# Performance work log

Hardware: AMD Instinct MI355X
Metric: run time of the kernel (lower is better)

Reference implementation:

```python
import jax, jax.numpy as jnp
import numpy as np
from jax.scipy.special import erf

# ---- physical constants (scipy.constants values; FIELD_CONSTANT in eV*Angstrom per e^2) ----
E_CHARGE = 1.602176634e-19
EPS0 = 8.8541878128e-12
PI = float(np.pi)
FIELD_CONSTANT = E_CHARGE * 1e10 / EPS0          # e/(eps0) with Angstrom length units
K_COUL = FIELD_CONSTANT / (4.0 * PI)             # ~14.3996 eV*A

# ---- module hyperparameters (from init_kwargs) ----
SIGMA_D = 0.5
SIGMAS = np.array([0.4, 0.8, 1.2, 1.6], dtype=np.float32)
NUM_RADIAL = 4
OFFSET = 0.1
N_PER_GRAPH = 128
NUM_GRAPHS = 32
M_NODES = N_PER_GRAPH * NUM_GRAPHS

# total_width_factors = sqrt((sigma_d^2 + sigma_r^2)/2)
W_FACTORS = np.sqrt((SIGMA_D**2 + SIGMAS**2) / 2.0).astype(np.float32)      # [R]
# multipole-normalized GTO: C_l = 1/(2^{l+1/2} sigma^{2l+3} Gamma(l+3/2)) => C1/C0 = 1/(3 sigma^2)
L0_FACTORS = np.ones(NUM_RADIAL, dtype=np.float32)                          # ratio = 1 under 'multipoles'
L1_FACTORS = (np.sqrt(3.0) * SIGMAS**2 * (1.0 / (3.0 * SIGMAS**2)) / OFFSET).astype(np.float32)

# 7 duplicate offsets: center, +x, +y, +z, -x, -y, -z
_h = OFFSET
OFFSETS7 = np.array([[0,0,0],[_h,0,0],[0,_h,0],[0,0,_h],[-_h,0,0],[0,-_h,0],[0,0,-_h]], dtype=np.float32)


def _duplicate_charges(sf):
    # sf: [M,4] -> [M,7] FD charge assignment (matches torch slot layout)
    t = 2.0 * OFFSET
    s0, s1, s2, s3 = sf[:, 0], sf[:, 1], sf[:, 2], sf[:, 3]
    return jnp.stack([s0, s3 / t, s1 / t, s2 / t, -s3 / t, -s1 / t, -s2 / t], axis=1)


def _project(sf7):
    # sf7: [M,7,R] per-duplicate scalar features -> [M, 4R]
    M = sf7.shape[0]
    l0 = jnp.asarray(L0_FACTORS) * sf7[:, 0]                                 # [M,R]
    half = 0.5 * jnp.asarray(L1_FACTORS)
    vy = half * (sf7[:, 2] - sf7[:, 5])   # column offset 0 in each triplet
    vz = half * (sf7[:, 3] - sf7[:, 6])   # column offset 1
    vx = half * (sf7[:, 1] - sf7[:, 4])   # column offset 2
    l1 = jnp.stack([vy, vz, vx], axis=-1).reshape(M, 3 * NUM_RADIAL)         # interleaved per radial
    return jnp.concatenate([l0, l1], axis=1)                                 # [M,4R]


def setup_inputs() -> dict:
    key = jax.random.key(0)
    k1, k2 = jax.random.split(key)
    source_feats = jax.random.normal(k1, (M_NODES, 1, 4), dtype=jnp.float32)
    node_positions = 4.0 * jax.random.normal(k2, (M_NODES, 3), dtype=jnp.float32)  # ~Angstrom scale
    batch = jnp.repeat(jnp.arange(NUM_GRAPHS, dtype=jnp.int64), N_PER_GRAPH)
    return {"source_feats": source_feats, "node_positions": node_positions, "batch": batch}


def reference(source_feats, node_positions, batch):
    # density_max_l=1, projection_max_l=1 -> call_density_1_feats_1 path.
    # Assumes equal-size graphs: batch = repeat(arange(G), n) (enforced by setup_inputs).
    sf = source_feats[:, 0, :]                                               # squeeze(-2): [M,4]
    M = sf.shape[0]
    G, n, D, R = NUM_GRAPHS, N_PER_GRAPH, 7 * N_PER_GRAPH, NUM_RADIAL
    w = jnp.asarray(W_FACTORS)                                               # [R]

    charges = _duplicate_charges(sf)                                         # [M,7]
    pos7 = node_positions[:, None, :] + jnp.asarray(OFFSETS7)[None]          # [M,7,3]

    pg = pos7.reshape(G, D, 3)
    cg = charges.reshape(G, D)

    diff = pg[:, :, None, :] - pg[:, None, :, :]                             # [G,D,D,3]
    d2 = jnp.sum(diff * diff, axis=-1)                                       # [G,D,D]
    orig = jnp.arange(D) // 7
    mask = (orig[:, None] != orig[None, :])                                  # exclude same-original-node pairs
    d = jnp.sqrt(jnp.where(mask, d2, 1.0))                                   # safe sqrt (masked entries dummy)
    smooth = erf(0.5 * d[..., None] / w) / (d[..., None] + 1e-6)             # [G,D,D,R]
    smooth = smooth * mask[None, :, :, None]
    # scatter_sum over senders i into receivers j
    sfeat = K_COUL * jnp.einsum('gi,gijr->gjr', cg, smooth)                  # [G,D,R]
    sfeat = sfeat.reshape(M, 7, R)

    # GTOSelfInteractionBlock (reconstructed): interactions among a node's own
    # 7 duplicates with analytic d->0 limit erf(x)/x -> 1/(w*sqrt(pi)).
    off = jnp.asarray(OFFSETS7)
    ds = jnp.linalg.norm(off[:, None, :] - off[None, :, :], axis=-1)          # [7,7]
    phi = jnp.where(ds[..., None] > 0.0,
                    erf(0.5 * ds[..., None] / w) / (ds[..., None] + 1e-6),
                    1.0 / (w * np.sqrt(PI)))                                  # [7,7,R]
    sself = K_COUL * jnp.einsum('mi,ijr->mjr', charges, phi)                  # [M,7,R]

    features = _project(sfeat)
    self_terms = _project(sself)
    features = features + self_terms                                          # include_self_interaction=True
    return features, self_terms
```

## Files before the change

kernel.cpp:

```cpp
#include <hip/hip_runtime.h>
#include <math.h>

namespace {

constexpr int   MTOT = 4096;
constexpr float H    = 0.1f;

constexpr float W0 = 0.45276925690687087f;
constexpr float W1 = 0.66708320320631664f;
constexpr float W2 = 0.91923881554251174f;
constexpr float W3 = 1.18532695911296985f;

constexpr float KCOUL   = 14.399645478425669f;
constexpr float HALF_L1 = 2.8867513459481287f;
constexpr float SQRTPI  = 1.7724538509055159f;
constexpr float TWOSQPI = 1.1283791670955126f;

constexpr float K0 = 1.1043153f, K1 = 0.74953184f, K2 = 0.54392830f, K3 = 0.42182454f;

constexpr float PK0 = 0.5195472f, PK1 = 0.3526314f, PK2 = 0.2559019f, PK3 = 0.1984558f;
constexpr float C20 = -1.7593842f, C21 = -0.8105028f, C22 = -0.4268329f, C23 = -0.2567073f;
constexpr float EA1 = 0.3480242f, EA2 = -0.0958798f, EA3 = 0.7478556f;
constexpr float RCP_H = 9.9999000f, RCP_HS2 = 7.0710178f, RCP_2H = 4.9999750f;

constexpr int   TABN  = 512;
constexpr float TAB_H = 0.015f;
constexpr float INV_H = 66.666664f;

constexpr int   TGN   = 256;
constexpr float TG_H  = 0.03f;
constexpr float INV_G = 33.333332f;

constexpr float NEAR2 = 4.0f;
constexpr float SAT2  = 49.4f;

__device__ __forceinline__ float fast_rcp(float x)  { return __builtin_amdgcn_rcpf(x); }
__device__ __forceinline__ float fast_rsq(float x)  { return __builtin_amdgcn_rsqf(x); }
__device__ __forceinline__ float fast_exp2(float x) { return __builtin_amdgcn_exp2f(x); }

__device__ __forceinline__ float erf_q(float d, float d2, float pk, float c2) {
  float t = fast_rcp(__builtin_fmaf(d, pk, 1.0f));
  float poly = t * __builtin_fmaf(t, __builtin_fmaf(t, EA3, EA2), EA1);
  return poly * fast_exp2(d2 * c2);
}

__device__ __forceinline__ float project_one(const float* S, int k) {
  if (k < 4) return S[k];
  int q = k - 4;
  int r = q / 3;
  int comp = q - 3 * r;
  int j1, j2;
  if (comp == 0)      { j1 = 2; j2 = 5; }
  else if (comp == 1) { j1 = 3; j2 = 6; }
  else                { j1 = 1; j2 = 4; }
  return HALF_L1 * (S[j1 * 4 + r] - S[j2 * 4 + r]);
}

__device__ __forceinline__ unsigned spread3(int v) {
  return (unsigned)((v & 1) | ((v & 2) << 2) | ((v & 4) << 4));
}

__global__ __launch_bounds__(896, 4) void es_main(
    const float* __restrict__ sf,
    const float* __restrict__ pos,
    float* __restrict__ out)
{
  __shared__ float4   s_pos4[128];
  __shared__ float4   s_chg4[128];
  __shared__ int      s_orig[128];
  __shared__ unsigned s_key[128];
  __shared__ float4   s_tabV[TABN];
  __shared__ float4   s_tabD[TABN];
  __shared__ float4   s_gV[TGN], s_gD[TGN];
  __shared__ float4   s_tV[TGN], s_tD[TGN];
  __shared__ __align__(16) char s_u[8 * 112 * 16];
  __shared__ float    s_feat[448];
  __shared__ float    s_self[448];

  float (*s_tmp)[TABN + 1] = reinterpret_cast<float (*)[TABN + 1]>(s_u);
  float4* s_part = reinterpret_cast<float4*>(s_u);

  const int b   = blockIdx.x;
  const int g   = b >> 3;
  const int nb  = b & 7;
  const int tid = threadIdx.x;

  float px = 0.f, py = 0.f, pz = 0.f;
  float4 myc = make_float4(0.f, 0.f, 0.f, 0.f);
  if (tid < 128) {
    const float* p = pos + (size_t)(g * 128 + tid) * 3;
    px = p[0]; py = p[1]; pz = p[2];
    const float4 s = ((const float4*)sf)[g * 128 + tid];
    myc = make_float4(s.x, 5.0f * s.w, 5.0f * s.y, 5.0f * s.z);
    int cx = (int)((px + 16.0f) * 0.25f); cx = (cx < 0) ? 0 : (cx > 7 ? 7 : cx);
    int cy = (int)((py + 16.0f) * 0.25f); cy = (cy < 0) ? 0 : (cy > 7 ? 7 : cy);
    int cz = (int)((pz + 16.0f) * 0.25f); cz = (cz < 0) ? 0 : (cz > 7 ? 7 : cz);
    unsigned mort = spread3(cx) | (spread3(cy) << 1) | (spread3(cz) << 2);
    s_key[tid] = (mort << 7) | (unsigned)tid;
  }
  if (tid <= TABN) {
    const float d = tid * TAB_H;
    s_tmp[0][tid] = erff(K0 * d);
    s_tmp[1][tid] = erff(K1 * d);
    s_tmp[2][tid] = erff(K2 * d);
    s_tmp[3][tid] = erff(K3 * d);
  }
  if (tid >= 640) {
    const int e = tid - 640;
    const float d0 = fmaxf(e * TG_H, 1e-3f);
    const float d1 = (e + 1) * TG_H;
    const float ks[4] = {K0, K1, K2, K3};
    float gv[4], gd[4], tv[4], td[4];
#pragma unroll
    for (int r = 0; r < 4; ++r) {
      const float k = ks[r];
      const float e0 = erff(k * d0), e1 = erff(k * d1);
      const float x0 = expf(-k * k * d0 * d0), x1 = expf(-k * k * d1 * d1);
      const float g0 = e0 / d0, g1 = e1 / d1;
      const float t0 = 0.2f * e0 / (d0 * d0 * d0) - 0.2f * TWOSQPI * k * x0 / (d0 * d0);
      const float t1 = 0.2f * e1 / (d1 * d1 * d1) - 0.2f * TWOSQPI * k * x1 / (d1 * d1);
      gv[r] = g0; gd[r] = g1 - g0; tv[r] = t0; td[r] = t1 - t0;
    }
    s_gV[e] = make_float4(gv[0], gv[1], gv[2], gv[3]);
    s_gD[e] = make_float4(gd[0], gd[1], gd[2], gd[3]);
    s_tV[e] = make_float4(tv[0], tv[1], tv[2], tv[3]);
    s_tD[e] = make_float4(td[0], td[1], td[2], td[3]);
  }
  __syncthreads();

  if (tid < 128) {
    const unsigned mykey = s_key[tid];
    int rank = 0;
    for (int t = 0; t < 128; ++t) rank += (s_key[t] < mykey) ? 1 : 0;
    s_pos4[rank] = make_float4(px, py, pz, 0.0f);
    s_chg4[rank] = myc;
    s_orig[rank] = tid;
  }
  if (tid < TABN) {
    const float v0 = s_tmp[0][tid], v1 = s_tmp[1][tid];
    const float v2v = s_tmp[2][tid], v3 = s_tmp[3][tid];
    s_tabV[tid] = make_float4(v0, v1, v2v, v3);
    s_tabD[tid] = make_float4(s_tmp[0][tid + 1] - v0, s_tmp[1][tid + 1] - v1,
                              s_tmp[2][tid + 1] - v2v, s_tmp[3][tid + 1] - v3);
  }
  __syncthreads();

  const int site_local = tid % 112;
  const int chunk      = tid / 112;
  const int sl   = nb * 112 + site_local;
  const int jown = (sl * 9363) >> 16;
  const int aoff = sl - jown * 7;

  const float4 cp = s_pos4[jown];
  const float tx = cp.x + ((aoff == 1) ? H : (aoff == 4) ? -H : 0.0f);
  const float ty = cp.y + ((aoff == 2) ? H : (aoff == 5) ? -H : 0.0f);
  const float tz = cp.z + ((aoff == 3) ? H : (aoff == 6) ? -H : 0.0f);

  float a0 = 0.f, a1 = 0.f, a2 = 0.f, a3 = 0.f, Ssat = 0.f;

  auto acc_full = [&](float d2raw, float c) {
    float d2 = fmaxf(d2raw, 1e-12f);
    float rd = fast_rsq(d2);
    float cv = c * rd;
    float t  = (d2 * rd) * INV_H;
    int  idx = (int)t;
    float f  = t - (float)idx;
    idx = (idx < TABN - 1) ? idx : (TABN - 1);
    f = fminf(f, 1.0f);
    const float4 V = s_tabV[idx];
    const float4 D = s_tabD[idx];
    a0 = __builtin_fmaf(cv, __builtin_fmaf(D.x, f, V.x), a0);
    a1 = __builtin_fmaf(cv, __builtin_fmaf(D.y, f, V.y), a1);
    a2 = __builtin_fmaf(cv, __builtin_fmaf(D.z, f, V.z), a2);
    a3 = __builtin_fmaf(cv, __builtin_fmaf(D.w, f, V.w), a3);
  };

  const int j0 = chunk * 16;
  for (int jj = 0; jj < 16; ++jj) {
    const int j = j0 + jj;
    const float4 p4 = s_pos4[j];
    const float4 c4 = s_chg4[j];
    const float vx = tx - p4.x;
    const float vy = ty - p4.y;
    const float vz = tz - p4.z;
    const float v2 = __builtin_fmaf(vx, vx, __builtin_fmaf(vy, vy, vz * vz));
    if (__any(v2 < NEAR2)) {
      const float w2 = v2 + 0.01f;
      const bool own = (j == jown);
      acc_full(v2,                            (own & (aoff == 0)) ? 0.0f :  c4.x);
      acc_full(__builtin_fmaf(vx, -0.2f, w2), (own & (aoff == 1)) ? 0.0f :  c4.y);
      acc_full(__builtin_fmaf(vy, -0.2f, w2), (own & (aoff == 2)) ? 0.0f :  c4.z);
      acc_full(__builtin_fmaf(vz, -0.2f, w2), (own & (aoff == 3)) ? 0.0f :  c4.w);
      acc_full(__builtin_fmaf(vx,  0.2f, w2), (own & (aoff == 4)) ? 0.0f : -c4.y);
      acc_full(__builtin_fmaf(vy,  0.2f, w2), (own & (aoff == 5)) ? 0.0f : -c4.z);
      acc_full(__builtin_fmaf(vz,  0.2f, w2), (own & (aoff == 6)) ? 0.0f : -c4.w);
    } else if (__any(v2 < SAT2)) {
      const float rd  = fast_rsq(v2);
      const float d   = v2 * rd;
      const float dot = __builtin_fmaf(c4.y, vx, __builtin_fmaf(c4.z, vy, c4.w * vz));
      const float t   = d * INV_G;
      const int   idx = (int)t;
      const bool  in  = (idx < TGN - 1);
      const int   ic  = in ? idx : (TGN - 2);
      const float f   = fminf(t - (float)idx, 1.0f);
      const float4 Gv = s_gV[ic], Gd = s_gD[ic];
      const float4 Tv = s_tV[ic], Td = s_tD[ic];
      const float rd2 = rd * rd;
      const float gs  = rd;
      const float ts  = 0.2f * rd2 * rd;
      const float g0v = in ? __builtin_fmaf(Gd.x, f, Gv.x) : gs;
      const float g1v = in ? __builtin_fmaf(Gd.y, f, Gv.y) : gs;
      const float g2v = in ? __builtin_fmaf(Gd.z, f, Gv.z) : gs;
      const float g3v = in ? __builtin_fmaf(Gd.w, f, Gv.w) : gs;
      const float t0v = in ? __builtin_fmaf(Td.x, f, Tv.x) : ts;
      const float t1v = in ? __builtin_fmaf(Td.y, f, Tv.y) : ts;
      const float t2v = in ? __builtin_fmaf(Td.z, f, Tv.z) : ts;
      const float t3v = in ? __builtin_fmaf(Td.w, f, Tv.w) : ts;
      a0 = __builtin_fmaf(c4.x, g0v, __builtin_fmaf(dot, t0v, a0));
      a1 = __builtin_fmaf(c4.x, g1v, __builtin_fmaf(dot, t1v, a1));
      a2 = __builtin_fmaf(c4.x, g2v, __builtin_fmaf(dot, t2v, a2));
      a3 = __builtin_fmaf(c4.x, g3v, __builtin_fmaf(dot, t3v, a3));
    } else {
      const float rd  = fast_rsq(v2);
      const float dot = __builtin_fmaf(c4.y, vx, __builtin_fmaf(c4.z, vy, c4.w * vz));
      Ssat = __builtin_fmaf(c4.x, rd, Ssat);
      Ssat = __builtin_fmaf(0.2f * dot, rd * rd * rd, Ssat);
    }
  }
  a0 += Ssat; a1 += Ssat; a2 += Ssat; a3 += Ssat;

  s_part[chunk * 112 + site_local] = make_float4(a0, a1, a2, a3);
  __syncthreads();

  if (tid < 448) {
    const int site = tid >> 2;
    const int r    = tid & 3;
    const float* pf = (const float*)s_part;
    float tot = 0.f;
#pragma unroll
    for (int c = 0; c < 8; ++c) tot += pf[c * 448 + tid];

    const float w  = (r == 0) ? W0  : (r == 1) ? W1  : (r == 2) ? W2  : W3;
    const float pk = (r == 0) ? PK0 : (r == 1) ? PK1 : (r == 2) ? PK2 : PK3;
    const float c2 = (r == 0) ? C20 : (r == 1) ? C21 : (r == 2) ? C22 : C23;
    const float diag = fast_rcp(w * SQRTPI);
    const float ph1 = (1.f - erf_q(0.1f,        0.01f, pk, c2)) * RCP_H;
    const float ph2 = (1.f - erf_q(0.14142136f, 0.02f, pk, c2)) * RCP_HS2;
    const float ph3 = (1.f - erf_q(0.2f,        0.04f, pk, c2)) * RCP_2H;

    const int jn = (site * 9363) >> 16;
    const int ba = site - jn * 7;
    const float4 c4 = s_chg4[nb * 16 + jn];
    float selfSum = 0.f, ca = 0.f;
#pragma unroll
    for (int i = 0; i < 7; ++i) {
      const float ci = (i == 0) ?  c4.x : (i == 1) ?  c4.y : (i == 2) ?  c4.z :
                       (i == 3) ?  c4.w : (i == 4) ? -c4.y : (i == 5) ? -c4.z : -c4.w;
      float ph;
      if (i == ba)                             ph = diag;
      else if (i == 0 || ba == 0)              ph = ph1;
      else if ((i - ba == 3) || (ba - i == 3)) ph = ph3;
      else                                     ph = ph2;
      selfSum = __builtin_fmaf(ci, ph, selfSum);
      if (i == ba) ca = ci;
    }
    s_self[tid] = KCOUL * selfSum;
    s_feat[tid] = KCOUL * __builtin_fmaf(ca, diag, tot);
  }
  __syncthreads();

  if (tid < 256) {
    const int node = tid >> 4;
    const int k    = tid & 15;
    const int m    = g * 128 + s_orig[nb * 16 + node];
    float vf = project_one(&s_feat[node * 28], k);
    float vs = project_one(&s_self[node * 28], k);
    out[m * 16 + k]             = vf;
    out[MTOT * 16 + m * 16 + k] = vs;
  }
}

}

extern "C" void kernel_launch(void* const* d_in, const int* in_sizes, int n_in,
                              void* d_out, int out_size, void* d_ws, size_t ws_size,
                              hipStream_t stream) {
  const float* sf  = (const float*)d_in[0];
  const float* pos = (const float*)d_in[1];
  float* out = (float*)d_out;
  es_main<<<256, 896, 0, stream>>>(sf, pos, out);
}
```

Before: 70.34 us.

## Evaluate multipole table for all pairs, then correct near pairs exactly

Replaces the three-way branch per neighbor (near, mid, saturated) with a branch-free pass that applies the tabulated monopole+dipole approximation to every pair. It records a wave-uniform near mask and afterwards revisits only the near pairs, subtracting the approximate term and adding the exact 7-duplicate evaluation. Table construction now uses Taylor series for small distances so the table is valid down to zero. This removes divergent branching and allows unrolling, at the cost of extra table lookups for far pairs, recomputation for near pairs, and possible cancellation error from the subtract-then-add.

```diff
diff --git a/kernel.cpp b/kernel.cpp
--- a/kernel.cpp
+++ b/kernel.cpp
@@ -32,7 +32,6 @@
 constexpr float INV_G = 33.333332f;
 
 constexpr float NEAR2 = 4.0f;
-constexpr float SAT2  = 49.4f;
 
 __device__ __forceinline__ float fast_rcp(float x)  { return __builtin_amdgcn_rcpf(x); }
 __device__ __forceinline__ float fast_rsq(float x)  { return __builtin_amdgcn_rsqf(x); }
@@ -42,6 +41,21 @@
   float t = fast_rcp(__builtin_fmaf(d, pk, 1.0f));
   float poly = t * __builtin_fmaf(t, __builtin_fmaf(t, EA3, EA2), EA1);
   return poly * fast_exp2(d2 * c2);
+}
+
+__device__ __forceinline__ float g_of(float k, float d) {
+  const float k2d2 = k * k * d * d;
+  if (d < 0.5f)
+    return TWOSQPI * k * (1.0f - k2d2 * (1.0f / 3.0f) + k2d2 * k2d2 * 0.1f);
+  return erff(k * d) / d;
+}
+__device__ __forceinline__ float gt_of(float k, float d) {
+  const float k2d2 = k * k * d * d;
+  if (d < 0.5f)
+    return 0.2f * TWOSQPI * k * k * k *
+           (2.0f / 3.0f - 0.4f * k2d2 + k2d2 * k2d2 * (1.0f / 7.0f));
+  const float e = erff(k * d), x = expf(-k2d2);
+  return 0.2f * e / (d * d * d) - 0.2f * TWOSQPI * k * x / (d * d);
 }
 
 __device__ __forceinline__ float project_one(const float* S, int k) {
@@ -107,18 +121,15 @@
   }
   if (tid >= 640) {
     const int e = tid - 640;
-    const float d0 = fmaxf(e * TG_H, 1e-3f);
+    const float d0 = e * TG_H;
     const float d1 = (e + 1) * TG_H;
     const float ks[4] = {K0, K1, K2, K3};
     float gv[4], gd[4], tv[4], td[4];
 #pragma unroll
     for (int r = 0; r < 4; ++r) {
       const float k = ks[r];
-      const float e0 = erff(k * d0), e1 = erff(k * d1);
-      const float x0 = expf(-k * k * d0 * d0), x1 = expf(-k * k * d1 * d1);
-      const float g0 = e0 / d0, g1 = e1 / d1;
-      const float t0 = 0.2f * e0 / (d0 * d0 * d0) - 0.2f * TWOSQPI * k * x0 / (d0 * d0);
-      const float t1 = 0.2f * e1 / (d1 * d1 * d1) - 0.2f * TWOSQPI * k * x1 / (d1 * d1);
+      const float g0 = g_of(k, d0),  g1 = g_of(k, d1);
+      const float t0 = gt_of(k, d0), t1 = gt_of(k, d1);
       gv[r] = g0; gd[r] = g1 - g0; tv[r] = t0; td[r] = t1 - t0;
     }
     s_gV[e] = make_float4(gv[0], gv[1], gv[2], gv[3]);
@@ -156,7 +167,42 @@
   const float ty = cp.y + ((aoff == 2) ? H : (aoff == 5) ? -H : 0.0f);
   const float tz = cp.z + ((aoff == 3) ? H : (aoff == 6) ? -H : 0.0f);
 
-  float a0 = 0.f, a1 = 0.f, a2 = 0.f, a3 = 0.f, Ssat = 0.f;
+  float a0 = 0.f, a1 = 0.f, a2 = 0.f, a3 = 0.f;
+
+  auto mid_contrib = [&](int j, float& v2raw) -> float4 {
+    const float4 p4 = s_pos4[j];
+    const float4 c4 = s_chg4[j];
+    const float vx = tx - p4.x;
+    const float vy = ty - p4.y;
+    const float vz = tz - p4.z;
+    const float v2r = __builtin_fmaf(vx, vx, __builtin_fmaf(vy, vy, vz * vz));
+    v2raw = v2r;
+    const float v2 = fmaxf(v2r, 1e-6f);
+    const float rd = fast_rsq(v2);
+    const float d  = v2 * rd;
+    const float dot = __builtin_fmaf(c4.y, vx, __builtin_fmaf(c4.z, vy, c4.w * vz));
+    const float t   = d * INV_G;
+    const int   idx = (int)t;
+    const bool  in  = (idx < TGN - 1);
+    const int   ic  = in ? idx : (TGN - 2);
+    const float f   = fminf(t - (float)idx, 1.0f);
+    const float4 Gv = s_gV[ic], Gd = s_gD[ic];
+    const float4 Tv = s_tV[ic], Td = s_tD[ic];
+    const float gs  = rd;
+    const float ts  = 0.2f * rd * rd * rd;
+    const float g0v = in ? __builtin_fmaf(Gd.x, f, Gv.x) : gs;
+    const float g1v = in ? __builtin_fmaf(Gd.y, f, Gv.y) : gs;
+    const float g2v = in ? __builtin_fmaf(Gd.z, f, Gv.z) : gs;
+    const float g3v = in ? __builtin_fmaf(Gd.w, f, Gv.w) : gs;
+    const float t0v = in ? __builtin_fmaf(Td.x, f, Tv.x) : ts;
+    const float t1v = in ? __builtin_fmaf(Td.y, f, Tv.y) : ts;
+    const float t2v = in ? __builtin_fmaf(Td.z, f, Tv.z) : ts;
+    const float t3v = in ? __builtin_fmaf(Td.w, f, Tv.w) : ts;
+    return make_float4(__builtin_fmaf(c4.x, g0v, dot * t0v),
+                       __builtin_fmaf(c4.x, g1v, dot * t1v),
+                       __builtin_fmaf(c4.x, g2v, dot * t2v),
+                       __builtin_fmaf(c4.x, g3v, dot * t3v));
+  };
 
   auto acc_full = [&](float d2raw, float c) {
     float d2 = fmaxf(d2raw, 1e-12f);
@@ -176,58 +222,39 @@
   };
 
   const int j0 = chunk * 16;
+
+  unsigned nearmask = 0;
+#pragma unroll 4
   for (int jj = 0; jj < 16; ++jj) {
+    float v2r;
+    const float4 r = mid_contrib(j0 + jj, v2r);
+    a0 += r.x; a1 += r.y; a2 += r.z; a3 += r.w;
+    if (__any(v2r < NEAR2)) nearmask |= (1u << jj);
+  }
+
+  while (nearmask) {
+    const int jj = __ffs(nearmask) - 1;
+    nearmask &= nearmask - 1;
     const int j = j0 + jj;
+    float v2r;
+    const float4 r = mid_contrib(j, v2r);
+    a0 -= r.x; a1 -= r.y; a2 -= r.z; a3 -= r.w;
     const float4 p4 = s_pos4[j];
     const float4 c4 = s_chg4[j];
     const float vx = tx - p4.x;
     const float vy = ty - p4.y;
     const float vz = tz - p4.z;
     const float v2 = __builtin_fmaf(vx, vx, __builtin_fmaf(vy, vy, vz * vz));
-    if (__any(v2 < NEAR2)) {
-      const float w2 = v2 + 0.01f;
-      const bool own = (j == jown);
-      acc_full(v2,                            (own & (aoff == 0)) ? 0.0f :  c4.x);
-      acc_full(__builtin_fmaf(vx, -0.2f, w2), (own & (aoff == 1)) ? 0.0f :  c4.y);
-      acc_full(__builtin_fmaf(vy, -0.2f, w2), (own & (aoff == 2)) ? 0.0f :  c4.z);
-      acc_full(__builtin_fmaf(vz, -0.2f, w2), (own & (aoff == 3)) ? 0.0f :  c4.w);
-      acc_full(__builtin_fmaf(vx,  0.2f, w2), (own & (aoff == 4)) ? 0.0f : -c4.y);
-      acc_full(__builtin_fmaf(vy,  0.2f, w2), (own & (aoff == 5)) ? 0.0f : -c4.z);
-      acc_full(__builtin_fmaf(vz,  0.2f, w2), (own & (aoff == 6)) ? 0.0f : -c4.w);
-    } else if (__any(v2 < SAT2)) {
-      const float rd  = fast_rsq(v2);
-      const float d   = v2 * rd;
-      const float dot = __builtin_fmaf(c4.y, vx, __builtin_fmaf(c4.z, vy, c4.w * vz));
-      const float t   = d * INV_G;
-      const int   idx = (int)t;
-      const bool  in  = (idx < TGN - 1);
-      const int   ic  = in ? idx : (TGN - 2);
-      const float f   = fminf(t - (float)idx, 1.0f);
-      const float4 Gv = s_gV[ic], Gd = s_gD[ic];
-      const float4 Tv = s_tV[ic], Td = s_tD[ic];
-      const float rd2 = rd * rd;
-      const float gs  = rd;
-      const float ts  = 0.2f * rd2 * rd;
-      const float g0v = in ? __builtin_fmaf(Gd.x, f, Gv.x) : gs;
-      const float g1v = in ? __builtin_fmaf(Gd.y, f, Gv.y) : gs;
-      const float g2v = in ? __builtin_fmaf(Gd.z, f, Gv.z) : gs;
-      const float g3v = in ? __builtin_fmaf(Gd.w, f, Gv.w) : gs;
-      const float t0v = in ? __builtin_fmaf(Td.x, f, Tv.x) : ts;
-      const float t1v = in ? __builtin_fmaf(Td.y, f, Tv.y) : ts;
-      const float t2v = in ? __builtin_fmaf(Td.z, f, Tv.z) : ts;
-      const float t3v = in ? __builtin_fmaf(Td.w, f, Tv.w) : ts;
-      a0 = __builtin_fmaf(c4.x, g0v, __builtin_fmaf(dot, t0v, a0));
-      a1 = __builtin_fmaf(c4.x, g1v, __builtin_fmaf(dot, t1v, a1));
-      a2 = __builtin_fmaf(c4.x, g2v, __builtin_fmaf(dot, t2v, a2));
-      a3 = __builtin_fmaf(c4.x, g3v, __builtin_fmaf(dot, t3v, a3));
-    } else {
-      const float rd  = fast_rsq(v2);
-      const float dot = __builtin_fmaf(c4.y, vx, __builtin_fmaf(c4.z, vy, c4.w * vz));
-      Ssat = __builtin_fmaf(c4.x, rd, Ssat);
-      Ssat = __builtin_fmaf(0.2f * dot, rd * rd * rd, Ssat);
-    }
-  }
-  a0 += Ssat; a1 += Ssat; a2 += Ssat; a3 += Ssat;
+    const float w2 = v2 + 0.01f;
+    const bool own = (j == jown);
+    acc_full(v2,                            (own & (aoff == 0)) ? 0.0f :  c4.x);
+    acc_full(__builtin_fmaf(vx, -0.2f, w2), (own & (aoff == 1)) ? 0.0f :  c4.y);
+    acc_full(__builtin_fmaf(vy, -0.2f, w2), (own & (aoff == 2)) ? 0.0f :  c4.z);
+    acc_full(__builtin_fmaf(vz, -0.2f, w2), (own & (aoff == 3)) ? 0.0f :  c4.w);
+    acc_full(__builtin_fmaf(vx,  0.2f, w2), (own & (aoff == 4)) ? 0.0f : -c4.y);
+    acc_full(__builtin_fmaf(vy,  0.2f, w2), (own & (aoff == 5)) ? 0.0f : -c4.z);
+    acc_full(__builtin_fmaf(vz,  0.2f, w2), (own & (aoff == 6)) ? 0.0f : -c4.w);
+  }
 
   s_part[chunk * 112 + site_local] = make_float4(a0, a1, a2, a3);
   __syncthreads();
```

Result: slower. 77.12 us (+9.6%).

## Split into prep and main kernels, replace near-field erf table with inline approximation

Applied to the files above, without the earlier changes.

A separate prep kernel now builds the far-field interpolation tables and the Morton-sorted positions, charges and original indices once per graph, writing them to workspace. The main kernel launches four times as many smaller blocks (448 threads, 28 sites each) that copy these precomputed tables from global memory instead of recomputing erf tables per block. Near-field erf lookups are replaced by an inline rational-exp erf approximation, and the small-distance table entries use Taylor series. The intent is to remove redundant per-block table setup and raise parallelism, at the cost of an extra launch, global round trips and more ALU work in the near-field path. An empty leftover conditional remains in the code.

```diff
diff --git a/kernel.cpp b/kernel.cpp
--- a/kernel.cpp
+++ b/kernel.cpp
@@ -23,16 +23,14 @@
 constexpr float EA1 = 0.3480242f, EA2 = -0.0958798f, EA3 = 0.7478556f;
 constexpr float RCP_H = 9.9999000f, RCP_HS2 = 7.0710178f, RCP_2H = 4.9999750f;
 
-constexpr int   TABN  = 512;
-constexpr float TAB_H = 0.015f;
-constexpr float INV_H = 66.666664f;
-
 constexpr int   TGN   = 256;
 constexpr float TG_H  = 0.03f;
 constexpr float INV_G = 33.333332f;
 
 constexpr float NEAR2 = 4.0f;
-constexpr float SAT2  = 49.4f;
+
+constexpr int WS_GRAPH_BASE = 1024;
+constexpr int WS_ORIG_F4    = 9216;
 
 __device__ __forceinline__ float fast_rcp(float x)  { return __builtin_amdgcn_rcpf(x); }
 __device__ __forceinline__ float fast_rsq(float x)  { return __builtin_amdgcn_rsqf(x); }
@@ -42,6 +40,21 @@
   float t = fast_rcp(__builtin_fmaf(d, pk, 1.0f));
   float poly = t * __builtin_fmaf(t, __builtin_fmaf(t, EA3, EA2), EA1);
   return poly * fast_exp2(d2 * c2);
+}
+
+__device__ __forceinline__ float g_of(float k, float d) {
+  const float k2d2 = k * k * d * d;
+  if (d < 0.5f)
+    return TWOSQPI * k * (1.0f - k2d2 * (1.0f / 3.0f) + k2d2 * k2d2 * 0.1f);
+  return erff(k * d) / d;
+}
+__device__ __forceinline__ float gt_of(float k, float d) {
+  const float k2d2 = k * k * d * d;
+  if (d < 0.5f)
+    return 0.2f * TWOSQPI * k * k * k *
+           (2.0f / 3.0f - 0.4f * k2d2 + k2d2 * k2d2 * (1.0f / 7.0f));
+  const float e = erff(k * d), x = expf(-k2d2);
+  return 0.2f * e / (d * d * d) - 0.2f * TWOSQPI * k * x / (d * d);
 }
 
 __device__ __forceinline__ float project_one(const float* S, int k) {
@@ -60,31 +73,34 @@
   return (unsigned)((v & 1) | ((v & 2) << 2) | ((v & 4) << 4));
 }
 
-__global__ __launch_bounds__(896, 4) void es_main(
-    const float* __restrict__ sf,
-    const float* __restrict__ pos,
-    float* __restrict__ out)
+__global__ __launch_bounds__(256) void es_prep(
+    const float* __restrict__ sf, const float* __restrict__ pos,
+    float4* __restrict__ ws4, int* __restrict__ wsOrig)
 {
-  __shared__ float4   s_pos4[128];
-  __shared__ float4   s_chg4[128];
-  __shared__ int      s_orig[128];
+  const int b   = blockIdx.x;
+  const int tid = threadIdx.x;
+
+  if (b == 0) {
+    const float d0 = tid * TG_H;
+    const float d1 = (tid + 1) * TG_H;
+    const float ks[4] = {K0, K1, K2, K3};
+    float gv[4], gd[4], tv[4], td[4];
+#pragma unroll
+    for (int r = 0; r < 4; ++r) {
+      const float k  = ks[r];
+      const float g0 = g_of(k, d0),  g1 = g_of(k, d1);
+      const float t0 = gt_of(k, d0), t1 = gt_of(k, d1);
+      gv[r] = g0; gd[r] = g1 - g0; tv[r] = t0; td[r] = t1 - t0;
+    }
+    ws4[tid]       = make_float4(gv[0], gv[1], gv[2], gv[3]);
+    ws4[256 + tid] = make_float4(gd[0], gd[1], gd[2], gd[3]);
+    ws4[512 + tid] = make_float4(tv[0], tv[1], tv[2], tv[3]);
+    ws4[768 + tid] = make_float4(td[0], td[1], td[2], td[3]);
+    return;
+  }
+
   __shared__ unsigned s_key[128];
-  __shared__ float4   s_tabV[TABN];
-  __shared__ float4   s_tabD[TABN];
-  __shared__ float4   s_gV[TGN], s_gD[TGN];
-  __shared__ float4   s_tV[TGN], s_tD[TGN];
-  __shared__ __align__(16) char s_u[8 * 112 * 16];
-  __shared__ float    s_feat[448];
-  __shared__ float    s_self[448];
-
-  float (*s_tmp)[TABN + 1] = reinterpret_cast<float (*)[TABN + 1]>(s_u);
-  float4* s_part = reinterpret_cast<float4*>(s_u);
-
-  const int b   = blockIdx.x;
-  const int g   = b >> 3;
-  const int nb  = b & 7;
-  const int tid = threadIdx.x;
-
+  const int g = b - 1;
   float px = 0.f, py = 0.f, pz = 0.f;
   float4 myc = make_float4(0.f, 0.f, 0.f, 0.f);
   if (tid < 128) {
@@ -98,56 +114,45 @@
     unsigned mort = spread3(cx) | (spread3(cy) << 1) | (spread3(cz) << 2);
     s_key[tid] = (mort << 7) | (unsigned)tid;
   }
-  if (tid <= TABN) {
-    const float d = tid * TAB_H;
-    s_tmp[0][tid] = erff(K0 * d);
-    s_tmp[1][tid] = erff(K1 * d);
-    s_tmp[2][tid] = erff(K2 * d);
-    s_tmp[3][tid] = erff(K3 * d);
-  }
-  if (tid >= 640) {
-    const int e = tid - 640;
-    const float d0 = fmaxf(e * TG_H, 1e-3f);
-    const float d1 = (e + 1) * TG_H;
-    const float ks[4] = {K0, K1, K2, K3};
-    float gv[4], gd[4], tv[4], td[4];
-#pragma unroll
-    for (int r = 0; r < 4; ++r) {
-      const float k = ks[r];
-      const float e0 = erff(k * d0), e1 = erff(k * d1);
-      const float x0 = expf(-k * k * d0 * d0), x1 = expf(-k * k * d1 * d1);
-      const float g0 = e0 / d0, g1 = e1 / d1;
-      const float t0 = 0.2f * e0 / (d0 * d0 * d0) - 0.2f * TWOSQPI * k * x0 / (d0 * d0);
-      const float t1 = 0.2f * e1 / (d1 * d1 * d1) - 0.2f * TWOSQPI * k * x1 / (d1 * d1);
-      gv[r] = g0; gd[r] = g1 - g0; tv[r] = t0; td[r] = t1 - t0;
-    }
-    s_gV[e] = make_float4(gv[0], gv[1], gv[2], gv[3]);
-    s_gD[e] = make_float4(gd[0], gd[1], gd[2], gd[3]);
-    s_tV[e] = make_float4(tv[0], tv[1], tv[2], tv[3]);
-    s_tD[e] = make_float4(td[0], td[1], td[2], td[3]);
-  }
-  __syncthreads();
-
+  __syncthreads();
   if (tid < 128) {
     const unsigned mykey = s_key[tid];
     int rank = 0;
     for (int t = 0; t < 128; ++t) rank += (s_key[t] < mykey) ? 1 : 0;
-    s_pos4[rank] = make_float4(px, py, pz, 0.0f);
-    s_chg4[rank] = myc;
-    s_orig[rank] = tid;
-  }
-  if (tid < TABN) {
-    const float v0 = s_tmp[0][tid], v1 = s_tmp[1][tid];
-    const float v2v = s_tmp[2][tid], v3 = s_tmp[3][tid];
-    s_tabV[tid] = make_float4(v0, v1, v2v, v3);
-    s_tabD[tid] = make_float4(s_tmp[0][tid + 1] - v0, s_tmp[1][tid + 1] - v1,
-                              s_tmp[2][tid + 1] - v2v, s_tmp[3][tid + 1] - v3);
-  }
-  __syncthreads();
-
-  const int site_local = tid % 112;
-  const int chunk      = tid / 112;
-  const int sl   = nb * 112 + site_local;
+    ws4[WS_GRAPH_BASE + g * 256 + rank]       = make_float4(px, py, pz, 0.0f);
+    ws4[WS_GRAPH_BASE + g * 256 + 128 + rank] = myc;
+    wsOrig[g * 128 + rank] = tid;
+  }
+}
+
+__global__ __launch_bounds__(448, 7) void es_main(
+    const float4* __restrict__ ws4, const int* __restrict__ wsOrig,
+    float* __restrict__ out)
+{
+  __shared__ float4 s_tabs[1024];
+  __shared__ float4 s_pos4[128];
+  __shared__ float4 s_chg4[128];
+  __shared__ int    s_orig[128];
+  __shared__ float4 s_part[448];
+  __shared__ float  s_feat[112];
+  __shared__ float  s_self[112];
+
+  const int b   = blockIdx.x;
+  const int g   = b >> 5;
+  const int sb  = b & 31;
+  const int tid = threadIdx.x;
+
+  for (int i = tid; i < 1024; i += 448) s_tabs[i] = ws4[i];
+  if (tid < 128) {
+    s_pos4[tid] = ws4[WS_GRAPH_BASE + g * 256 + tid];
+    s_chg4[tid] = ws4[WS_GRAPH_BASE + g * 256 + 128 + tid];
+    s_orig[tid] = wsOrig[g * 128 + tid];
+  }
+  __syncthreads();
+
+  const int site_local = tid % 28;
+  const int chunk      = tid / 28;
+  const int sl   = sb * 28 + site_local;
   const int jown = (sl * 9363) >> 16;
   const int aoff = sl - jown * 7;
 
@@ -161,22 +166,17 @@
   auto acc_full = [&](float d2raw, float c) {
     float d2 = fmaxf(d2raw, 1e-12f);
     float rd = fast_rsq(d2);
+    float d  = d2 * rd;
     float cv = c * rd;
-    float t  = (d2 * rd) * INV_H;
-    int  idx = (int)t;
-    float f  = t - (float)idx;
-    idx = (idx < TABN - 1) ? idx : (TABN - 1);
-    f = fminf(f, 1.0f);
-    const float4 V = s_tabV[idx];
-    const float4 D = s_tabD[idx];
-    a0 = __builtin_fmaf(cv, __builtin_fmaf(D.x, f, V.x), a0);
-    a1 = __builtin_fmaf(cv, __builtin_fmaf(D.y, f, V.y), a1);
-    a2 = __builtin_fmaf(cv, __builtin_fmaf(D.z, f, V.z), a2);
-    a3 = __builtin_fmaf(cv, __builtin_fmaf(D.w, f, V.w), a3);
+    a0 = __builtin_fmaf(cv, 1.0f - erf_q(d, d2, PK0, C20), a0);
+    a1 = __builtin_fmaf(cv, 1.0f - erf_q(d, d2, PK1, C21), a1);
+    a2 = __builtin_fmaf(cv, 1.0f - erf_q(d, d2, PK2, C22), a2);
+    a3 = __builtin_fmaf(cv, 1.0f - erf_q(d, d2, PK3, C23), a3);
   };
 
-  const int j0 = chunk * 16;
-  for (int jj = 0; jj < 16; ++jj) {
+  const int j0 = chunk * 8;
+#pragma unroll
+  for (int jj = 0; jj < 8; ++jj) {
     const int j = j0 + jj;
     const float4 p4 = s_pos4[j];
     const float4 c4 = s_chg4[j];
@@ -194,51 +194,54 @@
       acc_full(__builtin_fmaf(vx,  0.2f, w2), (own & (aoff == 4)) ? 0.0f : -c4.y);
       acc_full(__builtin_fmaf(vy,  0.2f, w2), (own & (aoff == 5)) ? 0.0f : -c4.z);
       acc_full(__builtin_fmaf(vz,  0.2f, w2), (own & (aoff == 6)) ? 0.0f : -c4.w);
-    } else if (__any(v2 < SAT2)) {
-      const float rd  = fast_rsq(v2);
-      const float d   = v2 * rd;
-      const float dot = __builtin_fmaf(c4.y, vx, __builtin_fmaf(c4.z, vy, c4.w * vz));
-      const float t   = d * INV_G;
-      const int   idx = (int)t;
-      const bool  in  = (idx < TGN - 1);
-      const int   ic  = in ? idx : (TGN - 2);
-      const float f   = fminf(t - (float)idx, 1.0f);
-      const float4 Gv = s_gV[ic], Gd = s_gD[ic];
-      const float4 Tv = s_tV[ic], Td = s_tD[ic];
-      const float rd2 = rd * rd;
-      const float gs  = rd;
-      const float ts  = 0.2f * rd2 * rd;
-      const float g0v = in ? __builtin_fmaf(Gd.x, f, Gv.x) : gs;
-      const float g1v = in ? __builtin_fmaf(Gd.y, f, Gv.y) : gs;
-      const float g2v = in ? __builtin_fmaf(Gd.z, f, Gv.z) : gs;
-      const float g3v = in ? __builtin_fmaf(Gd.w, f, Gv.w) : gs;
-      const float t0v = in ? __builtin_fmaf(Td.x, f, Tv.x) : ts;
-      const float t1v = in ? __builtin_fmaf(Td.y, f, Tv.y) : ts;
-      const float t2v = in ? __builtin_fmaf(Td.z, f, Tv.z) : ts;
-      const float t3v = in ? __builtin_fmaf(Td.w, f, Tv.w) : ts;
-      a0 = __builtin_fmaf(c4.x, g0v, __builtin_fmaf(dot, t0v, a0));
-      a1 = __builtin_fmaf(c4.x, g1v, __builtin_fmaf(dot, t1v, a1));
-      a2 = __builtin_fmaf(c4.x, g2v, __builtin_fmaf(dot, t2v, a2));
-      a3 = __builtin_fmaf(c4.x, g3v, __builtin_fmaf(dot, t3v, a3));
     } else {
       const float rd  = fast_rsq(v2);
       const float dot = __builtin_fmaf(c4.y, vx, __builtin_fmaf(c4.z, vy, c4.w * vz));
-      Ssat = __builtin_fmaf(c4.x, rd, Ssat);
-      Ssat = __builtin_fmaf(0.2f * dot, rd * rd * rd, Ssat);
+      const float d   = v2 * rd;
+      if (d * INV_G < (float)(TGN - 1) ? __any(d * INV_G < (float)(TGN - 1)) : false) {
+      }
+      if (__any(v2 < 58.9f)) {
+        const float t   = d * INV_G;
+        const int   idx = (int)t;
+        const bool  in  = (idx < TGN - 1);
+        const int   ic  = in ? idx : (TGN - 2);
+        const float f   = fminf(t - (float)idx, 1.0f);
+        const float4 Gv = s_tabs[ic];
+        const float4 Gd = s_tabs[256 + ic];
+        const float4 Tv = s_tabs[512 + ic];
+        const float4 Td = s_tabs[768 + ic];
+        const float gs  = rd;
+        const float ts  = 0.2f * rd * rd * rd;
+        const float g0v = in ? __builtin_fmaf(Gd.x, f, Gv.x) : gs;
+        const float g1v = in ? __builtin_fmaf(Gd.y, f, Gv.y) : gs;
+        const float g2v = in ? __builtin_fmaf(Gd.z, f, Gv.z) : gs;
+        const float g3v = in ? __builtin_fmaf(Gd.w, f, Gv.w) : gs;
+        const float t0v = in ? __builtin_fmaf(Td.x, f, Tv.x) : ts;
+        const float t1v = in ? __builtin_fmaf(Td.y, f, Tv.y) : ts;
+        const float t2v = in ? __builtin_fmaf(Td.z, f, Tv.z) : ts;
+        const float t3v = in ? __builtin_fmaf(Td.w, f, Tv.w) : ts;
+        a0 = __builtin_fmaf(c4.x, g0v, __builtin_fmaf(dot, t0v, a0));
+        a1 = __builtin_fmaf(c4.x, g1v, __builtin_fmaf(dot, t1v, a1));
+        a2 = __builtin_fmaf(c4.x, g2v, __builtin_fmaf(dot, t2v, a2));
+        a3 = __builtin_fmaf(c4.x, g3v, __builtin_fmaf(dot, t3v, a3));
+      } else {
+        Ssat = __builtin_fmaf(c4.x, rd, Ssat);
+        Ssat = __builtin_fmaf(0.2f * dot, rd * rd * rd, Ssat);
+      }
     }
   }
   a0 += Ssat; a1 += Ssat; a2 += Ssat; a3 += Ssat;
 
-  s_part[chunk * 112 + site_local] = make_float4(a0, a1, a2, a3);
-  __syncthreads();
-
-  if (tid < 448) {
+  s_part[chunk * 28 + site_local] = make_float4(a0, a1, a2, a3);
+  __syncthreads();
+
+  if (tid < 112) {
     const int site = tid >> 2;
     const int r    = tid & 3;
     const float* pf = (const float*)s_part;
     float tot = 0.f;
 #pragma unroll
-    for (int c = 0; c < 8; ++c) tot += pf[c * 448 + tid];
+    for (int c = 0; c < 16; ++c) tot += pf[c * 112 + tid];
 
     const float w  = (r == 0) ? W0  : (r == 1) ? W1  : (r == 2) ? W2  : W3;
     const float pk = (r == 0) ? PK0 : (r == 1) ? PK1 : (r == 2) ? PK2 : PK3;
@@ -250,7 +253,7 @@
 
     const int jn = (site * 9363) >> 16;
     const int ba = site - jn * 7;
-    const float4 c4 = s_chg4[nb * 16 + jn];
+    const float4 c4 = s_chg4[sb * 4 + jn];
     float selfSum = 0.f, ca = 0.f;
 #pragma unroll
     for (int i = 0; i < 7; ++i) {
@@ -269,12 +272,12 @@
   }
   __syncthreads();
 
-  if (tid < 256) {
-    const int node = tid >> 4;
-    const int k    = tid & 15;
-    const int m    = g * 128 + s_orig[nb * 16 + node];
-    float vf = project_one(&s_feat[node * 28], k);
-    float vs = project_one(&s_self[node * 28], k);
+  if (tid < 64) {
+    const int nl = tid >> 4;
+    const int k  = tid & 15;
+    const int m  = g * 128 + s_orig[sb * 4 + nl];
+    float vf = project_one(&s_feat[nl * 28], k);
+    float vs = project_one(&s_self[nl * 28], k);
     out[m * 16 + k]             = vf;
     out[MTOT * 16 + m * 16 + k] = vs;
   }
@@ -287,6 +290,9 @@
                               hipStream_t stream) {
   const float* sf  = (const float*)d_in[0];
   const float* pos = (const float*)d_in[1];
-  float* out = (float*)d_out;
-  es_main<<<256, 896, 0, stream>>>(sf, pos, out);
-}
+  float*  out    = (float*)d_out;
+  float4* ws4    = (float4*)d_ws;
+  int*    wsOrig = (int*)((char*)d_ws + (size_t)WS_ORIG_F4 * 16);
+  es_prep<<<33, 256, 0, stream>>>(sf, pos, ws4, wsOrig);
+  es_main<<<1024, 448, 0, stream>>>(ws4, wsOrig, out);
+}
```

Result: slower. 78.02 us (+10.9%).
